# Optimization experiments

Measured on AMD Instinct MI355X. Metric: run time of the kernel, lower is better.

## Reference

```python
import jax, jax.numpy as jnp
import numpy as np

C = 512
K = 3
DIL = 1
EPS = 1e-6


def weight_quant(w):
    # BitNet b1.58 ternary quantization with straight-through estimator:
    # scale = mean(|w|); w_q = clamp(round(w/scale), -1, 1) * scale
    s = jnp.maximum(jnp.mean(jnp.abs(w)), 1e-5)
    q = jnp.clip(jnp.round(w / s), -1.0, 1.0) * s
    return w + jax.lax.stop_gradient(q - w)


def conv1d(x, w, b, padding, dilation):
    # x: [B, C, L], w: [O, I, K]
    y = jax.lax.conv_general_dilated(
        x, w, window_strides=(1,), padding=[(padding, padding)],
        rhs_dilation=(dilation,), dimension_numbers=("NCH", "OIH", "NCH"))
    return y + b[None, :, None]


def setup_inputs() -> dict:
    key = jax.random.key(0)
    k0, k1, k2, k3, k4 = jax.random.split(key, 5)
    fan_in = C * K
    lim = 1.0 / np.sqrt(fan_in)
    x = jax.random.normal(k0, (16, C, 4096), dtype=jnp.float32)
    w1 = jax.random.uniform(k1, (C, C, K), jnp.float32, -lim, lim)
    b1 = jax.random.uniform(k2, (C,), jnp.float32, -lim, lim)
    w2 = jax.random.uniform(k3, (C, C, K), jnp.float32, -lim, lim)
    b2 = jax.random.uniform(k4, (C,), jnp.float32, -lim, lim)
    g = jnp.ones((C,), dtype=jnp.float32)  # RMSNorm gain
    return {"x": x, "w1": w1, "b1": b1, "w2": w2, "b2": b2, "g": g}


def reference(x, w1, b1, w2, b2, g):
    residual = x
    # RMSNorm over channel axis (original transposes to [B,L,C], norms last dim)
    ms = jnp.mean(jnp.square(x), axis=1, keepdims=True)
    h = x * jax.lax.rsqrt(ms + EPS) * g[None, :, None]
    h = jax.nn.silu(h)
    p1 = (K * DIL - DIL) // 2
    h = conv1d(h, weight_quant(w1), b1, p1, DIL)
    h = jax.nn.silu(h)
    h = conv1d(h, weight_quant(w2), b2, K // 2, 1)
    return h + residual
```

## Files before the change

kernel.cpp:

```cpp
#include <hip/hip_runtime.h>

#define BATCH 16
#define CCH 512
#define LEN 4096
#define LPAD 4098

typedef unsigned short u16;
typedef __bf16 bf16x8 __attribute__((ext_vector_type(8)));
typedef float f32x4 __attribute__((ext_vector_type(4)));
typedef u16 u16x8 __attribute__((ext_vector_type(8)));
typedef u16 u16x4 __attribute__((ext_vector_type(4)));

__device__ __forceinline__ u16 f2bf(float f) {
    unsigned u = __float_as_uint(f);
    u = (u + 0x7fffu + ((u >> 16) & 1u)) >> 16;
    return (u16)u;
}
__device__ __forceinline__ float bf2f(u16 v) {
    return __uint_as_float(((unsigned)v) << 16);
}
__device__ __forceinline__ float silu_f(float v) {
    return v / (1.f + __expf(-v));
}
__device__ __forceinline__ void async16(const u16* g, u16* l) {
    __builtin_amdgcn_global_load_lds(
        (const __attribute__((address_space(1))) unsigned int*)g,
        (__attribute__((address_space(3))) unsigned int*)l, 16, 0, 0);
}

#define SBAR() __builtin_amdgcn_sched_barrier(0)
#define HWBAR() { SBAR(); __builtin_amdgcn_s_barrier(); SBAR(); }
#define WAIT_LGKM0() { asm volatile("s_waitcnt lgkmcnt(0)" ::: "memory"); SBAR(); }
#define WAIT_VM(n) { asm volatile("s_waitcnt vmcnt(" #n ")" ::: "memory"); SBAR(); }

__global__ __launch_bounds__(256)
void absmean_partial(const float* __restrict__ w1, const float* __restrict__ w2,
                     float* __restrict__ part) {
    const int tid = threadIdx.x;
    const int base = blockIdx.x * 3072;
    float s1 = 0.f, s2 = 0.f;
    for (int i = tid; i < 3072; i += 256) {
        s1 += fabsf(w1[base + i]);
        s2 += fabsf(w2[base + i]);
    }
    __shared__ float r1[256], r2[256];
    r1[tid] = s1; r2[tid] = s2;
    __syncthreads();
    for (int off = 128; off > 0; off >>= 1) {
        if (tid < off) { r1[tid] += r1[tid + off]; r2[tid] += r2[tid + off]; }
        __syncthreads();
    }
    if (tid == 0) { part[blockIdx.x] = r1[0]; part[256 + blockIdx.x] = r2[0]; }
}

__global__ __launch_bounds__(256)
void finalize_scale(const float* __restrict__ part, float* __restrict__ sv) {
    const int tid = threadIdx.x;
    __shared__ float r1[256], r2[256];
    r1[tid] = part[tid]; r2[tid] = part[256 + tid];
    __syncthreads();
    for (int off = 128; off > 0; off >>= 1) {
        if (tid < off) { r1[tid] += r1[tid + off]; r2[tid] += r2[tid + off]; }
        __syncthreads();
    }
    if (tid == 0) {
        sv[0] = fmaxf(r1[0] * (1.f / 786432.f), 1e-5f);
        sv[1] = fmaxf(r2[0] * (1.f / 786432.f), 1e-5f);
    }
}

__global__ __launch_bounds__(256)
void quantize_both(const float* __restrict__ w1, const float* __restrict__ w2,
                   const float* __restrict__ sv,
                   u16* __restrict__ wq1, u16* __restrict__ wq2) {
    const int idx = blockIdx.x * 256 + threadIdx.x;
    const float s1 = sv[0], s2 = sv[1];
    const int o   = idx / 1536;
    const int rem = idx - o * 1536;
    const int i   = rem / 3;
    const int k   = rem - i * 3;
    const int dst = k * (CCH * CCH) + o * CCH + i;
    float q1 = fmaxf(-1.f, fminf(1.f, rintf(w1[idx] / s1)));
    float q2 = fmaxf(-1.f, fminf(1.f, rintf(w2[idx] / s2)));
    wq1[dst] = f2bf(q1);
    wq2[dst] = f2bf(q2);
}

__global__ __launch_bounds__(256)
void zero_pads(u16* __restrict__ h, u16* __restrict__ h1) {
    const int idx = blockIdx.x * 256 + threadIdx.x;
    const int b = idx >> 10;
    const int r = (idx >> 9) & 1;
    const int i = idx & 511;
    const size_t off = ((size_t)b * LPAD + (r ? (LPAD - 1) : 0)) * CCH + i;
    h[off] = 0;
    h1[off] = 0;
}

__global__ __launch_bounds__(256)
void rms_silu_transpose(const float* __restrict__ x, const float* __restrict__ g,
                        u16* __restrict__ h_t) {
    __shared__ u16   xt[CCH][33];
    __shared__ float red[8][32];
    __shared__ float rinv[32];
    const int tid = threadIdx.x;
    const int bb  = blockIdx.x >> 7;
    const int l0  = (blockIdx.x & 127) << 5;

    const size_t xbase = (size_t)bb * CCH * LEN + l0;
    {
        const int i_hi = tid >> 3;
        const int l4   = (tid & 7) << 2;
        #pragma unroll
        for (int it = 0; it < 16; ++it) {
            const int i = it * 32 + i_hi;
            const float4 v = *(const float4*)&x[xbase + (size_t)i * LEN + l4];
            xt[i][l4 + 0] = f2bf(v.x);
            xt[i][l4 + 1] = f2bf(v.y);
            xt[i][l4 + 2] = f2bf(v.z);
            xt[i][l4 + 3] = f2bf(v.w);
        }
    }
    __syncthreads();
    {
        const int l = tid & 31, seg = tid >> 5;
        const int ibeg = seg * 64;
        float ss = 0.f;
        #pragma unroll 8
        for (int i = ibeg; i < ibeg + 64; ++i) {
            const float v = bf2f(xt[i][l]);
            ss += v * v;
        }
        red[seg][l] = ss;
    }
    __syncthreads();
    if (tid < 32) {
        float tot = 0.f;
        #pragma unroll
        for (int k2 = 0; k2 < 8; ++k2) tot += red[k2][tid];
        rinv[tid] = rsqrtf(tot * (1.f / 512.f) + 1e-6f);
    }
    __syncthreads();
    {
        const int l  = tid >> 3;
        const int i0 = (tid & 7) << 6;
        const float ri = rinv[l];
        const size_t ob = ((size_t)bb * LPAD + l0 + l + 1) * CCH + i0;
        for (int ii = 0; ii < 64; ii += 8) {
            u16x8 ov;
            #pragma unroll
            for (int jj = 0; jj < 8; ++jj) {
                const int i = i0 + ii + jj;
                float v = bf2f(xt[i][l]) * ri * g[i];
                ov[jj] = f2bf(silu_f(v));
            }
            *(u16x8*)&h_t[ob + ii] = ov;
        }
    }
}

template<int EPI>
__global__ __launch_bounds__(1024)
void conv_gemm11(const u16* __restrict__ Bsrc, const u16* __restrict__ Wq,
                 const float* __restrict__ sptr, const float* __restrict__ bias,
                 const float* __restrict__ resid, u16* __restrict__ outb,
                 float* __restrict__ outf) {
    extern __shared__ u16 lds[];
    const int tid  = threadIdx.x;
    const int lane = tid & 63;
    const int wave = tid >> 6;
    const int wm = wave >> 2;
    const int wn = wave & 3;

    const int wgid = (blockIdx.x & 7) * 64 + (blockIdx.x >> 3);
    const int mt = wgid & 1;
    const int nt = wgid >> 1;
    const int o0 = mt << 8;
    const int bb = nt >> 4;
    const int l0 = (nt & 15) << 8;

    const int sr  = tid >> 3;
    const int scu = ((tid & 7) << 3) ^ ((sr & 7) << 3);
    const int sdst = tid << 3;

    const u16* aSrcBase = Wq + (size_t)o0 * CCH + scu;
    const u16* bSrcBase = Bsrc + ((size_t)bb * LPAD + l0) * CCH + scu;

    auto stage_full = [&](int pb, int ks2, int i02) {
        #pragma unroll
        for (int j = 0; j < 2; ++j) {
            const int r = j * 128 + sr;
            async16(aSrcBase + ks2 * (CCH * CCH) + r * CCH + i02,
                    &lds[pb * 32768 + j * 8192 + sdst]);
            async16(bSrcBase + (size_t)(r + ks2) * CCH + i02,
                    &lds[pb * 32768 + 16384 + j * 8192 + sdst]);
        }
    };

    const int swz = (lane & 7) << 3;
    const int c0 = ((lane >> 4) << 3) ^ swz;
    const int c1 = (((lane >> 4) << 3) + 32) ^ swz;
    const int aB = wm * 4096 + (lane & 15) * 64;
    const int bB = 16384 + wn * 4096 + (lane & 15) * 64;

    f32x4 acc[4][4];
    #pragma unroll
    for (int m = 0; m < 4; ++m)
        #pragma unroll
        for (int n = 0; n < 4; ++n)
            acc[m][n] = (f32x4){0.f, 0.f, 0.f, 0.f};

    stage_full(0, 0, 0);
    WAIT_VM(0);
    HWBAR();

    int ks = 0, i0 = 0;
    auto step = [&](int t, int cbase, int obase) {
        int ksn = ks + 1, i0n = i0;
        if (ksn == 3) { ksn = 0; i0n += 64; }
        if (t < 23) stage_full(obase ? 1 : 0, ksn, i0n);
        bf16x8 a0[4], b0[4], a1[4], b1[4];
        #pragma unroll
        for (int m = 0; m < 4; ++m)
            a0[m] = *(const bf16x8*)&lds[cbase + aB + m * 1024 + c0];
        #pragma unroll
        for (int n = 0; n < 4; ++n)
            b0[n] = *(const bf16x8*)&lds[cbase + bB + n * 1024 + c0];
        #pragma unroll
        for (int m = 0; m < 4; ++m)
            a1[m] = *(const bf16x8*)&lds[cbase + aB + m * 1024 + c1];
        #pragma unroll
        for (int n = 0; n < 4; ++n)
            b1[n] = *(const bf16x8*)&lds[cbase + bB + n * 1024 + c1];
        #pragma unroll
        for (int m = 0; m < 4; ++m)
            #pragma unroll
            for (int n = 0; n < 4; ++n)
                acc[m][n] = __builtin_amdgcn_mfma_f32_16x16x32_bf16(
                    a0[m], b0[n], acc[m][n], 0, 0, 0);
        #pragma unroll
        for (int m = 0; m < 4; ++m)
            #pragma unroll
            for (int n = 0; n < 4; ++n)
                acc[m][n] = __builtin_amdgcn_mfma_f32_16x16x32_bf16(
                    a1[m], b1[n], acc[m][n], 0, 0, 0);
        WAIT_LGKM0();
        if (t < 23) { WAIT_VM(0); }
        HWBAR();
        ks = ksn; i0 = i0n;
    };

    #pragma unroll 2
    for (int t = 0; t < 24; ++t) {
        if ((t & 1) == 0) step(t, 0, 1);
        else              step(t, 32768, 0);
    }

    const float sc = sptr[0];

    if (EPI == 1) {
        #pragma unroll
        for (int m = 0; m < 4; ++m) {
            const int o_loc = wm * 64 + m * 16 + ((lane >> 4) << 2);
            const int ob = o0 + o_loc;
            const float b0 = bias[ob + 0], b1 = bias[ob + 1];
            const float b2 = bias[ob + 2], b3 = bias[ob + 3];
            #pragma unroll
            for (int n = 0; n < 4; ++n) {
                const int l_loc = wn * 64 + n * 16 + (lane & 15);
                const f32x4 a = acc[m][n];
                u16x4 ov;
                ov[0] = f2bf(silu_f(sc * a[0] + b0));
                ov[1] = f2bf(silu_f(sc * a[1] + b1));
                ov[2] = f2bf(silu_f(sc * a[2] + b2));
                ov[3] = f2bf(silu_f(sc * a[3] + b3));
                char* p = (char*)lds + l_loc * 512 +
                          (((unsigned)(o_loc << 1)) ^ ((l_loc & 7) << 4));
                *(u16x4*)p = ov;
            }
        }
        __syncthreads();
        const int l_r = tid >> 2;
        const int oq  = (tid & 3) << 3;
        u16* gdst = outb + ((size_t)bb * LPAD + l0 + l_r + 1) * CCH + o0 + oq;
        char* srp = (char*)lds + l_r * 512;
        const int swz2 = (l_r & 7) << 4;
        #pragma unroll
        for (int c = 0; c < 8; ++c) {
            const uint4 v = *(const uint4*)(srp + (((oq << 1) + c * 64) ^ swz2));
            *(uint4*)(gdst + c * 32) = v;
        }
    } else {
        const int lbase = l0 + wn * 64 + (lane & 15);
        const int obase = o0 + wm * 64 + ((lane >> 4) << 2);
        #pragma unroll
        for (int m = 0; m < 4; ++m) {
            const int ob = obase + m * 16;
            #pragma unroll
            for (int n = 0; n < 4; ++n) {
                const int l = lbase + n * 16;
                const f32x4 a = acc[m][n];
                #pragma unroll
                for (int jj = 0; jj < 4; ++jj) {
                    const size_t idx = ((size_t)bb * CCH + (ob + jj)) * LEN + l;
                    outf[idx] = sc * a[jj] + bias[ob + jj] + resid[idx];
                }
            }
        }
    }
}

extern "C" void kernel_launch(void* const* d_in, const int* in_sizes, int n_in,
                              void* d_out, int out_size, void* d_ws, size_t ws_size,
                              hipStream_t stream) {
    const float* x  = (const float*)d_in[0];
    const float* w1 = (const float*)d_in[1];
    const float* b1 = (const float*)d_in[2];
    const float* w2 = (const float*)d_in[3];
    const float* b2 = (const float*)d_in[4];
    const float* g  = (const float*)d_in[5];
    float* out = (float*)d_out;

    char* ws = (char*)d_ws;
    float* sv   = (float*)ws;
    float* part = (float*)(ws + 256);
    u16* wq1   = (u16*)(ws + 4096);
    u16* wq2   = (u16*)(ws + 4096 + 1572864);
    u16* h_t   = (u16*)(ws + 4096 + 2 * 1572864);
    u16* h1_t  = (u16*)(ws + 4096 + 2 * 1572864 + 67141632);

    hipFuncSetAttribute((const void*)conv_gemm11<1>,
                        hipFuncAttributeMaxDynamicSharedMemorySize, 131072);
    hipFuncSetAttribute((const void*)conv_gemm11<2>,
                        hipFuncAttributeMaxDynamicSharedMemorySize, 131072);

    absmean_partial<<<dim3(256), dim3(256), 0, stream>>>(w1, w2, part);
    finalize_scale<<<dim3(1), dim3(256), 0, stream>>>(part, sv);
    quantize_both<<<dim3(3072), dim3(256), 0, stream>>>(w1, w2, sv, wq1, wq2);
    zero_pads<<<dim3(64), dim3(256), 0, stream>>>(h_t, h1_t);
    rms_silu_transpose<<<dim3(2048), dim3(256), 0, stream>>>(x, g, h_t);
    conv_gemm11<1><<<dim3(512), dim3(1024), 131072, stream>>>(h_t, wq1, sv, b1,
                                                              nullptr, h1_t, nullptr);
    conv_gemm11<2><<<dim3(512), dim3(1024), 131072, stream>>>(h1_t, wq2, sv + 1, b2,
                                                              x, nullptr, out);
}
```

Before: 379.2 us.

## Halve GEMM K-step to 32 and cut LDS to 64KB for two blocks per CU

The conv GEMM now stages K-chunks of 32 instead of 64 per step, running 48 double-buffered steps with a new 4-way XOR swizzle. This halves dynamic LDS from 128KB to 64KB, which could let two 1024-thread workgroups share a CU. MFMA sections are wrapped in s_setprio raises. The bf16 epilogue now writes out in two 128-row passes so it fits in the smaller LDS. The trade-off is twice as many barriers and waits per K, with less work between them.

```diff
diff --git a/kernel.cpp b/kernel.cpp
--- a/kernel.cpp
+++ b/kernel.cpp
@@ -161,7 +161,7 @@
 
 template<int EPI>
 __global__ __launch_bounds__(1024)
-void conv_gemm11(const u16* __restrict__ Bsrc, const u16* __restrict__ Wq,
+void conv_gemm13(const u16* __restrict__ Bsrc, const u16* __restrict__ Wq,
                  const float* __restrict__ sptr, const float* __restrict__ bias,
                  const float* __restrict__ resid, u16* __restrict__ outb,
                  float* __restrict__ outf) {
@@ -179,29 +179,22 @@
     const int bb = nt >> 4;
     const int l0 = (nt & 15) << 8;
 
-    const int sr  = tid >> 3;
-    const int scu = ((tid & 7) << 3) ^ ((sr & 7) << 3);
+    const int srow = tid >> 2;
+    const int scol = (((tid & 3) ^ (srow & 3)) << 3);
     const int sdst = tid << 3;
 
-    const u16* aSrcBase = Wq + (size_t)o0 * CCH + scu;
-    const u16* bSrcBase = Bsrc + ((size_t)bb * LPAD + l0) * CCH + scu;
+    const u16* aSrcBase = Wq + (size_t)(o0 + srow) * CCH + scol;
+    const u16* bSrcBase = Bsrc + ((size_t)bb * LPAD + l0 + srow) * CCH + scol;
 
     auto stage_full = [&](int pb, int ks2, int i02) {
-        #pragma unroll
-        for (int j = 0; j < 2; ++j) {
-            const int r = j * 128 + sr;
-            async16(aSrcBase + ks2 * (CCH * CCH) + r * CCH + i02,
-                    &lds[pb * 32768 + j * 8192 + sdst]);
-            async16(bSrcBase + (size_t)(r + ks2) * CCH + i02,
-                    &lds[pb * 32768 + 16384 + j * 8192 + sdst]);
-        }
+        async16(aSrcBase + ks2 * (CCH * CCH) + i02, &lds[pb * 16384 + sdst]);
+        async16(bSrcBase + (size_t)ks2 * CCH + i02,
+                &lds[pb * 16384 + 8192 + sdst]);
     };
 
-    const int swz = (lane & 7) << 3;
-    const int c0 = ((lane >> 4) << 3) ^ swz;
-    const int c1 = (((lane >> 4) << 3) + 32) ^ swz;
-    const int aB = wm * 4096 + (lane & 15) * 64;
-    const int bB = 16384 + wn * 4096 + (lane & 15) * 64;
+    const int cc = (((lane >> 4) ^ (lane & 3)) << 3);
+    const int aB = (wm * 64 + (lane & 15)) * 32 + cc;
+    const int bB = 8192 + (wn * 64 + (lane & 15)) * 32 + cc;
 
     f32x4 acc[4][4];
     #pragma unroll
@@ -215,80 +208,76 @@
     HWBAR();
 
     int ks = 0, i0 = 0;
-    auto step = [&](int t, int cbase, int obase) {
+    for (int t = 0; t < 48; ++t) {
+        const int cur = t & 1;
+        const int cb = cur * 16384;
         int ksn = ks + 1, i0n = i0;
-        if (ksn == 3) { ksn = 0; i0n += 64; }
-        if (t < 23) stage_full(obase ? 1 : 0, ksn, i0n);
-        bf16x8 a0[4], b0[4], a1[4], b1[4];
+        if (ksn == 3) { ksn = 0; i0n += 32; }
+        if (t < 47) stage_full(cur ^ 1, ksn, i0n);
+        bf16x8 ar[4], br[4];
         #pragma unroll
         for (int m = 0; m < 4; ++m)
-            a0[m] = *(const bf16x8*)&lds[cbase + aB + m * 1024 + c0];
+            ar[m] = *(const bf16x8*)&lds[cb + aB + m * 512];
         #pragma unroll
         for (int n = 0; n < 4; ++n)
-            b0[n] = *(const bf16x8*)&lds[cbase + bB + n * 1024 + c0];
-        #pragma unroll
-        for (int m = 0; m < 4; ++m)
-            a1[m] = *(const bf16x8*)&lds[cbase + aB + m * 1024 + c1];
-        #pragma unroll
-        for (int n = 0; n < 4; ++n)
-            b1[n] = *(const bf16x8*)&lds[cbase + bB + n * 1024 + c1];
+            br[n] = *(const bf16x8*)&lds[cb + bB + n * 512];
+        __builtin_amdgcn_s_setprio(1);
         #pragma unroll
         for (int m = 0; m < 4; ++m)
             #pragma unroll
             for (int n = 0; n < 4; ++n)
                 acc[m][n] = __builtin_amdgcn_mfma_f32_16x16x32_bf16(
-                    a0[m], b0[n], acc[m][n], 0, 0, 0);
-        #pragma unroll
-        for (int m = 0; m < 4; ++m)
-            #pragma unroll
-            for (int n = 0; n < 4; ++n)
-                acc[m][n] = __builtin_amdgcn_mfma_f32_16x16x32_bf16(
-                    a1[m], b1[n], acc[m][n], 0, 0, 0);
+                    ar[m], br[n], acc[m][n], 0, 0, 0);
+        __builtin_amdgcn_s_setprio(0);
         WAIT_LGKM0();
-        if (t < 23) { WAIT_VM(0); }
+        if (t < 47) { WAIT_VM(0); }
         HWBAR();
         ks = ksn; i0 = i0n;
-    };
-
-    #pragma unroll 2
-    for (int t = 0; t < 24; ++t) {
-        if ((t & 1) == 0) step(t, 0, 1);
-        else              step(t, 32768, 0);
     }
 
     const float sc = sptr[0];
 
     if (EPI == 1) {
         #pragma unroll
-        for (int m = 0; m < 4; ++m) {
-            const int o_loc = wm * 64 + m * 16 + ((lane >> 4) << 2);
-            const int ob = o0 + o_loc;
-            const float b0 = bias[ob + 0], b1 = bias[ob + 1];
-            const float b2 = bias[ob + 2], b3 = bias[ob + 3];
-            #pragma unroll
-            for (int n = 0; n < 4; ++n) {
-                const int l_loc = wn * 64 + n * 16 + (lane & 15);
-                const f32x4 a = acc[m][n];
-                u16x4 ov;
-                ov[0] = f2bf(silu_f(sc * a[0] + b0));
-                ov[1] = f2bf(silu_f(sc * a[1] + b1));
-                ov[2] = f2bf(silu_f(sc * a[2] + b2));
-                ov[3] = f2bf(silu_f(sc * a[3] + b3));
-                char* p = (char*)lds + l_loc * 512 +
-                          (((unsigned)(o_loc << 1)) ^ ((l_loc & 7) << 4));
-                *(u16x4*)p = ov;
+        for (int pass = 0; pass < 2; ++pass) {
+            if ((wn >> 1) == pass) {
+                #pragma unroll
+                for (int m = 0; m < 4; ++m) {
+                    const int o_loc = wm * 64 + m * 16 + ((lane >> 4) << 2);
+                    const int ob = o0 + o_loc;
+                    const float b0 = bias[ob + 0], b1 = bias[ob + 1];
+                    const float b2 = bias[ob + 2], b3 = bias[ob + 3];
+                    #pragma unroll
+                    for (int n = 0; n < 4; ++n) {
+                        const int l_loc = (wn & 1) * 64 + n * 16 + (lane & 15);
+                        const f32x4 a = acc[m][n];
+                        u16x4 ov;
+                        ov[0] = f2bf(silu_f(sc * a[0] + b0));
+                        ov[1] = f2bf(silu_f(sc * a[1] + b1));
+                        ov[2] = f2bf(silu_f(sc * a[2] + b2));
+                        ov[3] = f2bf(silu_f(sc * a[3] + b3));
+                        char* p = (char*)lds + l_loc * 512 +
+                                  (((unsigned)(o_loc << 1)) ^ ((l_loc & 7) << 4));
+                        *(u16x4*)p = ov;
+                    }
+                }
             }
-        }
-        __syncthreads();
-        const int l_r = tid >> 2;
-        const int oq  = (tid & 3) << 3;
-        u16* gdst = outb + ((size_t)bb * LPAD + l0 + l_r + 1) * CCH + o0 + oq;
-        char* srp = (char*)lds + l_r * 512;
-        const int swz2 = (l_r & 7) << 4;
-        #pragma unroll
-        for (int c = 0; c < 8; ++c) {
-            const uint4 v = *(const uint4*)(srp + (((oq << 1) + c * 64) ^ swz2));
-            *(uint4*)(gdst + c * 32) = v;
+            __syncthreads();
+            {
+                const int row = tid >> 3;
+                const int ch0 = tid & 7;
+                u16* gdst = outb +
+                    ((size_t)bb * LPAD + l0 + pass * 128 + row + 1) * CCH + o0;
+                char* srp = (char*)lds + row * 512;
+                const int swz2 = (row & 7) << 4;
+                #pragma unroll
+                for (int c = 0; c < 4; ++c) {
+                    const int slot = c * 8 + ch0;
+                    const uint4 v = *(const uint4*)(srp + ((slot * 16) ^ swz2));
+                    *(uint4*)(gdst + slot * 8) = v;
+                }
+            }
+            __syncthreads();
         }
     } else {
         const int lbase = l0 + wn * 64 + (lane & 15);
@@ -329,18 +318,18 @@
     u16* h_t   = (u16*)(ws + 4096 + 2 * 1572864);
     u16* h1_t  = (u16*)(ws + 4096 + 2 * 1572864 + 67141632);
 
-    hipFuncSetAttribute((const void*)conv_gemm11<1>,
-                        hipFuncAttributeMaxDynamicSharedMemorySize, 131072);
-    hipFuncSetAttribute((const void*)conv_gemm11<2>,
-                        hipFuncAttributeMaxDynamicSharedMemorySize, 131072);
+    hipFuncSetAttribute((const void*)conv_gemm13<1>,
+                        hipFuncAttributeMaxDynamicSharedMemorySize, 65536);
+    hipFuncSetAttribute((const void*)conv_gemm13<2>,
+                        hipFuncAttributeMaxDynamicSharedMemorySize, 65536);
 
     absmean_partial<<<dim3(256), dim3(256), 0, stream>>>(w1, w2, part);
     finalize_scale<<<dim3(1), dim3(256), 0, stream>>>(part, sv);
     quantize_both<<<dim3(3072), dim3(256), 0, stream>>>(w1, w2, sv, wq1, wq2);
     zero_pads<<<dim3(64), dim3(256), 0, stream>>>(h_t, h1_t);
     rms_silu_transpose<<<dim3(2048), dim3(256), 0, stream>>>(x, g, h_t);
-    conv_gemm11<1><<<dim3(512), dim3(1024), 131072, stream>>>(h_t, wq1, sv, b1,
-                                                              nullptr, h1_t, nullptr);
-    conv_gemm11<2><<<dim3(512), dim3(1024), 131072, stream>>>(h1_t, wq2, sv + 1, b2,
-                                                              x, nullptr, out);
-}
+    conv_gemm13<1><<<dim3(512), dim3(1024), 65536, stream>>>(h_t, wq1, sv, b1,
+                                                             nullptr, h1_t, nullptr);
+    conv_gemm13<2><<<dim3(512), dim3(1024), 65536, stream>>>(h1_t, wq2, sv + 1, b2,
+                                                             x, nullptr, out);
+}
```

Result: faster. 345.9 us (-8.8%).
